# Kernel tuning notes

Measured on AMD Instinct MI355X. Metric: run time of the kernel, lower is better.

Reference implementation:

```python
import jax, jax.numpy as jnp
import numpy as np

DN = ('NCHW', 'OIHW', 'NCHW')

def _convlstm_scan(x, W, b):
    """x: [S,B,Cin,H,W]; W: [4*Co, Cin+Co, 3, 3]; b: [4*Co]. Returns all h: [S,B,Co,H,W]."""
    S, B, Cin, H, Wd = x.shape
    Co = W.shape[0] // 4
    h0 = jnp.zeros((B, Co, H, Wd), x.dtype)
    c0 = jnp.zeros((B, Co, H, Wd), x.dtype)

    def step(carry, xt):
        h, c = carry
        z = jax.lax.conv_general_dilated(
            jnp.concatenate([xt, h], axis=1), W,
            window_strides=(1, 1), padding='SAME', dimension_numbers=DN)
        z = z + b[None, :, None, None]
        i, f, o, g = jnp.split(z, 4, axis=1)
        c = jax.nn.sigmoid(f) * c + jax.nn.sigmoid(i) * jnp.tanh(g)
        h = jax.nn.sigmoid(o) * jnp.tanh(c)
        return (h, c), h

    _, outs = jax.lax.scan(step, (h0, c0), x)
    return outs


def setup_inputs() -> dict:
    key = jax.random.key(0)
    k1, k2, k3 = jax.random.split(key, 3)
    S, B, C, H, W = 16, 4, 32, 128, 128
    Co = 32
    x = jax.random.normal(k1, (S, B, C, H, W), dtype=jnp.float32)
    Wf = jax.random.normal(k2, (4 * Co, C + Co, 3, 3), dtype=jnp.float32) * 0.05
    bf = jnp.zeros((4 * Co,), dtype=jnp.float32)
    Wb = jax.random.normal(k3, (4 * Co, C + Co, 3, 3), dtype=jnp.float32) * 0.05
    bb = jnp.zeros((4 * Co,), dtype=jnp.float32)
    return {"x": x, "Wf": Wf, "bf": bf, "Wb": Wb, "bb": bb}


def reference(x, Wf, bf, Wb, bb):
    fwd_outs = _convlstm_scan(x, Wf, bf)            # [S,B,Co,H,W]
    bwd_outs = _convlstm_scan(x[::-1], Wb, bb)      # [S,B,Co,H,W] (time-reversed input)
    # Faithful to source: backward outputs concatenated WITHOUT re-flipping.
    return jnp.concatenate([fwd_outs, bwd_outs], axis=2)  # [S,B,2*Co,H,W]
```

## Files before the change

kernel.cpp:

```cpp
#include <hip/hip_runtime.h>

#define S_ 16
#define B_ 4
#define H_ 128
#define W_ 128
#define HW_ (H_ * W_)
#define NPOS 324
#define TILE_ELEMS (NPOS * 32)

typedef __attribute__((ext_vector_type(8))) _Float16 half8;
typedef __attribute__((ext_vector_type(4))) float f32x4;

__device__ __forceinline__ float sigf(float x) { return 1.f / (1.f + __expf(-x)); }
__device__ __forceinline__ float tanhf_(float x) { return 2.f / (1.f + __expf(-2.f * x)) - 1.f; }

__device__ __forceinline__ void gl2lds16(const _Float16* g, _Float16* l) {
    __builtin_amdgcn_global_load_lds(
        (const __attribute__((address_space(1))) unsigned int*)g,
        (__attribute__((address_space(3))) unsigned int*)l, 16, 0, 0);
}

__global__ void prep_pack(const float* __restrict__ Wf, const float* __restrict__ Wb,
                          _Float16* __restrict__ wpk) {
    int id = blockIdx.x * 256 + threadIdx.x;
    if (id >= 18432) return;
    int l = id & 63;
    int nf = (id >> 6) & 7;
    int ks = (id >> 9) % 18;
    int d = id / 9216;
    const float* Wsrc = d ? Wb : Wf;
    int tap = ks >> 1, half = ks & 1;
    int dy = tap / 3, dx = tap - dy * 3;
    int co = nf * 16 + (l & 15);
    _Float16* dst = wpk + (size_t)d * 73728 + ((size_t)(ks * 8 + nf) * 64 + l) * 8;
#pragma unroll
    for (int e = 0; e < 8; ++e) {
        int ci = half * 32 + (l >> 4) * 8 + e;
        dst[e] = (_Float16)Wsrc[((co * 64 + ci) * 3 + dy) * 3 + dx];
    }
}

__global__ void prep_xtiles(const float* __restrict__ x, _Float16* __restrict__ xt) {
    int id = blockIdx.x * 256 + threadIdx.x;
    if (id >= 16 * 4 * 64 * NPOS * 4) return;
    int cb = id & 3;
    int u = id >> 2;
    int pos = u % NPOS;
    int v = u / NPOS;
    int tile = v & 63;
    v >>= 6;
    int b = v & 3;
    int ts = v >> 2;
    int r = pos / 18, cc = pos - r * 18;
    int gy = (tile >> 3) * 16 + r - 1;
    int gx = (tile & 7) * 16 + cc - 1;
    bool inb = ((unsigned)gy < 128u) && ((unsigned)gx < 128u);
    const float* g = x + ((size_t)(ts * 4 + b) * 32 + cb * 8) * HW_ + (size_t)gy * W_ + gx;
    half8 vv;
#pragma unroll
    for (int e = 0; e < 8; ++e)
        vv[e] = inb ? (_Float16)g[e * HW_] : (_Float16)0.f;
    *(half8*)(xt + (size_t)u * 32 + cb * 8) = vv;
}

__device__ __forceinline__ half8 lda(const _Float16* __restrict__ base, int m, int dy,
                                     int dx, int px, int kg, int wq) {
    return *(const half8*)(base + (size_t)(((wq * 4 + m + dy) * 18) + px + dx) * 32 + kg * 8);
}
__device__ __forceinline__ half8 ldb(const _Float16* __restrict__ bw, int ks, int nf, int lane) {
    return *(const half8*)(bw + (size_t)(ks * 8 + nf) * 512 + lane * 8);
}

__global__ __launch_bounds__(256, 2)
void convlstm_step(const _Float16* __restrict__ xtiles,
                   const _Float16* __restrict__ hin,
                   _Float16* __restrict__ hout,
                   const _Float16* __restrict__ wpk,
                   const float* __restrict__ biasf, const float* __restrict__ biasb,
                   float* __restrict__ cst, float* __restrict__ out, int t) {
    const int tile = blockIdx.x;
    const int dirb = blockIdx.y;
    const int dir = dirb >> 2, b = dirb & 3;
    const int ts = dir ? (S_ - 1 - t) : t;

    const _Float16* base_x = xtiles + ((size_t)(ts * 4 + b) * 64 + tile) * TILE_ELEMS;
    const _Float16* base_h = hin + ((size_t)dirb * 64 + tile) * TILE_ELEMS;
    _Float16* hob = hout + (size_t)dirb * 64 * TILE_ELEMS;
    const _Float16* bw = wpk + (size_t)dir * 73728;
    const float* bias = dir ? biasb : biasf;
    float* cbase = cst + (size_t)dirb * 32 * HW_;
    float* outp = out + ((size_t)(t * 4 + b) * 64 + dir * 32) * HW_;

    __shared__ alignas(16) _Float16 bsh[2][8][64][8];

    const int tid = threadIdx.x;
    const int lane = tid & 63, wq = tid >> 6;
    const int px = lane & 15, kg = lane >> 4;

    f32x4 acc[4][8];
#pragma unroll
    for (int m = 0; m < 4; ++m)
#pragma unroll
        for (int nf = 0; nf < 8; ++nf) acc[m][nf] = (f32x4)(0.f);

    if (t == 0) {
#pragma unroll 1
        for (int tap = 0; tap < 9; ++tap) {
            int dy = tap / 3, dx = tap - dy * 3;
            half8 a[4];
#pragma unroll
            for (int m = 0; m < 4; ++m) a[m] = lda(base_x, m, dy, dx, px, kg, wq);
#pragma unroll
            for (int nf = 0; nf < 8; ++nf) {
                half8 bb8 = ldb(bw, tap * 2, nf, lane);
#pragma unroll
                for (int m = 0; m < 4; ++m)
                    acc[m][nf] = __builtin_amdgcn_mfma_f32_16x16x32_f16(a[m], bb8, acc[m][nf], 0, 0, 0);
            }
        }
    } else {
        half8 aP[4], aQ[4];
        {
            const _Float16* gs = bw + ((size_t)(0 * 8 + wq * 2) * 64 + lane) * 8;
            gl2lds16(gs, &bsh[0][wq * 2][0][0]);
            gl2lds16(gs + 512, &bsh[0][wq * 2 + 1][0][0]);
#pragma unroll
            for (int m = 0; m < 4; ++m) aP[m] = lda(base_x, m, 0, 0, px, kg, wq);
        }

        auto body = [&](int ks, half8(&acur)[4], half8(&anxt)[4]) {
            __syncthreads();
            if (ks < 17) {
                const int ksn = ks + 1;
                const _Float16* gs = bw + ((size_t)(ksn * 8 + wq * 2) * 64 + lane) * 8;
                gl2lds16(gs, &bsh[ksn & 1][wq * 2][0][0]);
                gl2lds16(gs + 512, &bsh[ksn & 1][wq * 2 + 1][0][0]);
                const int tapn = ksn >> 1;
                const int dyn_ = tapn / 3, dxn = tapn - dyn_ * 3;
                const _Float16* an = (ksn & 1) ? base_h : base_x;
#pragma unroll
                for (int m = 0; m < 4; ++m) anxt[m] = lda(an, m, dyn_, dxn, px, kg, wq);
            }
            const _Float16* lb = &bsh[ks & 1][0][0][0];
#pragma unroll
            for (int nf = 0; nf < 8; ++nf) {
                half8 bb8 = *(const half8*)(lb + nf * 512 + lane * 8);
#pragma unroll
                for (int m = 0; m < 4; ++m)
                    acc[m][nf] = __builtin_amdgcn_mfma_f32_16x16x32_f16(acur[m], bb8, acc[m][nf], 0, 0, 0);
            }
        };
#pragma unroll 1
        for (int ks = 0; ks < 18; ks += 2) {
            body(ks, aP, aQ);
            body(ks + 1, aQ, aP);
        }
    }

    const int q0 = px;
    const int gx0 = (tile & 7) * 16, gy0 = (tile >> 3) * 16;
    const int tx = tile & 7, ty_ = tile >> 3;
    const int lx0 = kg * 4;

    float bI[2], bF[2], bO[2], bG[2];
#pragma unroll
    for (int qs = 0; qs < 2; ++qs) {
        bI[qs] = bias[qs * 16 + q0];
        bF[qs] = bias[32 + qs * 16 + q0];
        bO[qs] = bias[64 + qs * 16 + q0];
        bG[qs] = bias[96 + qs * 16 + q0];
    }
#pragma unroll
    for (int m = 0; m < 4; ++m) {
        const int ly = wq * 4 + m;
        const int gy = gy0 + ly;
#pragma unroll
        for (int qs = 0; qs < 2; ++qs) {
            const int q = qs * 16 + q0;
            f32x4 zi = acc[m][qs], zf = acc[m][2 + qs], zo = acc[m][4 + qs], zg = acc[m][6 + qs];
            size_t off = (size_t)q * HW_ + (size_t)gy * W_ + gx0 + lx0;
            f32x4 cold = (f32x4)(0.f);
            if (t) cold = *(const f32x4*)(cbase + off);
            f32x4 cn, hn;
#pragma unroll
            for (int r = 0; r < 4; ++r) {
                float I = sigf(zi[r] + bI[qs]);
                float F = sigf(zf[r] + bF[qs]);
                float O = sigf(zo[r] + bO[qs]);
                float G = tanhf_(zg[r] + bG[qs]);
                float cnr = F * cold[r] + I * G;
                cn[r] = cnr;
                hn[r] = O * tanhf_(cnr);
            }
            *(f32x4*)(cbase + off) = cn;
            *(f32x4*)(outp + off) = hn;
#pragma unroll
            for (int r = 0; r < 4; ++r) {
                _Float16 hh = (_Float16)hn[r];
                int lx = lx0 + r;
                hob[((size_t)tile) * TILE_ELEMS + (size_t)((ly + 1) * 18 + lx + 1) * 32 + q] = hh;
                bool Le = (lx == 0) && (tx > 0);
                bool Re = (lx == 15) && (tx < 7);
                bool Te = (ly == 0) && (ty_ > 0);
                bool Be = (ly == 15) && (ty_ < 7);
                if (Le) hob[((size_t)tile - 1) * TILE_ELEMS + (size_t)((ly + 1) * 18 + 17) * 32 + q] = hh;
                if (Re) hob[((size_t)tile + 1) * TILE_ELEMS + (size_t)((ly + 1) * 18 + 0) * 32 + q] = hh;
                if (Te) hob[((size_t)tile - 8) * TILE_ELEMS + (size_t)(17 * 18 + lx + 1) * 32 + q] = hh;
                if (Be) hob[((size_t)tile + 8) * TILE_ELEMS + (size_t)(0 * 18 + lx + 1) * 32 + q] = hh;
                if (Te && Le) hob[((size_t)tile - 9) * TILE_ELEMS + (size_t)(17 * 18 + 17) * 32 + q] = hh;
                if (Te && Re) hob[((size_t)tile - 7) * TILE_ELEMS + (size_t)(17 * 18 + 0) * 32 + q] = hh;
                if (Be && Le) hob[((size_t)tile + 7) * TILE_ELEMS + (size_t)(0 * 18 + 17) * 32 + q] = hh;
                if (Be && Re) hob[((size_t)tile + 9) * TILE_ELEMS + (size_t)(0 * 18 + 0) * 32 + q] = hh;
            }
        }
    }
}

extern "C" void kernel_launch(void* const* d_in, const int* in_sizes, int n_in,
                              void* d_out, int out_size, void* d_ws, size_t ws_size,
                              hipStream_t stream) {
    const float* x  = (const float*)d_in[0];
    const float* Wf = (const float*)d_in[1];
    const float* bf = (const float*)d_in[2];
    const float* Wb = (const float*)d_in[3];
    const float* bb = (const float*)d_in[4];
    float* out = (float*)d_out;
    char* ws = (char*)d_ws;

    const size_t OFF_WPK = 0;
    const size_t OFF_XT  = 327680;
    const size_t OFF_H0  = OFF_XT + 84934656;
    const size_t OFF_H1  = OFF_H0 + 10616832;
    const size_t OFF_C   = OFF_H1 + 10616832;

    _Float16* wpk = (_Float16*)(ws + OFF_WPK);
    _Float16* xt  = (_Float16*)(ws + OFF_XT);
    _Float16* hb[2] = { (_Float16*)(ws + OFF_H0), (_Float16*)(ws + OFF_H1) };
    float* cst = (float*)(ws + OFF_C);

    hipMemsetAsync(ws + OFF_H0, 0, 2u * 10616832u, stream);

    prep_pack<<<dim3(72), dim3(256), 0, stream>>>(Wf, Wb, wpk);
    prep_xtiles<<<dim3(20736), dim3(256), 0, stream>>>(x, xt);

    for (int t = 0; t < S_; ++t) {
        convlstm_step<<<dim3(64, 8), dim3(256), 0, stream>>>(
            xt, hb[(t + 1) & 1], hb[t & 1], wpk, bf, bb, cst, out, t);
    }
}
```

Baseline: 649.9 us.

## Process x and h halves per tap together, store cell state in fp16

The main loop now runs once per tap (9 iterations) instead of once per k-slice (18). Each iteration double-buffers both the x and h weight halves and loads both A operands, which halves the number of __syncthreads barriers. The cell state buffer changes from fp32 to fp16, halving its read/write traffic at the cost of precision in the recurrent c state. Nontemporal loads in the x packing and nontemporal stores of the output are added, and the larger LDS buffer and extra A registers may reduce occupancy.

Result: slower. 683.6 us (+5.2%).

```diff
diff --git a/kernel.cpp b/kernel.cpp
--- a/kernel.cpp
+++ b/kernel.cpp
@@ -9,6 +9,7 @@
 #define TILE_ELEMS (NPOS * 32)
 
 typedef __attribute__((ext_vector_type(8))) _Float16 half8;
+typedef __attribute__((ext_vector_type(4))) _Float16 half4;
 typedef __attribute__((ext_vector_type(4))) float f32x4;
 
 __device__ __forceinline__ float sigf(float x) { return 1.f / (1.f + __expf(-x)); }
@@ -59,7 +60,7 @@
     half8 vv;
 #pragma unroll
     for (int e = 0; e < 8; ++e)
-        vv[e] = inb ? (_Float16)g[e * HW_] : (_Float16)0.f;
+        vv[e] = inb ? (_Float16)__builtin_nontemporal_load(g + e * HW_) : (_Float16)0.f;
     *(half8*)(xt + (size_t)u * 32 + cb * 8) = vv;
 }
 
@@ -77,7 +78,8 @@
                    _Float16* __restrict__ hout,
                    const _Float16* __restrict__ wpk,
                    const float* __restrict__ biasf, const float* __restrict__ biasb,
-                   float* __restrict__ cst, float* __restrict__ out, int t) {
+                   _Float16* __restrict__ cst,
+                   float* __restrict__ out, int t) {
     const int tile = blockIdx.x;
     const int dirb = blockIdx.y;
     const int dir = dirb >> 2, b = dirb & 3;
@@ -88,10 +90,10 @@
     _Float16* hob = hout + (size_t)dirb * 64 * TILE_ELEMS;
     const _Float16* bw = wpk + (size_t)dir * 73728;
     const float* bias = dir ? biasb : biasf;
-    float* cbase = cst + (size_t)dirb * 32 * HW_;
+    _Float16* cbase = cst + (size_t)dirb * 32 * HW_;
     float* outp = out + ((size_t)(t * 4 + b) * 64 + dir * 32) * HW_;
 
-    __shared__ alignas(16) _Float16 bsh[2][8][64][8];
+    __shared__ alignas(16) _Float16 bsh[2][2][8][64][8];
 
     const int tid = threadIdx.x;
     const int lane = tid & 63, wq = tid >> 6;
@@ -119,41 +121,55 @@
             }
         }
     } else {
-        half8 aP[4], aQ[4];
+        half8 aP[2][4], aQ[2][4];
         {
-            const _Float16* gs = bw + ((size_t)(0 * 8 + wq * 2) * 64 + lane) * 8;
-            gl2lds16(gs, &bsh[0][wq * 2][0][0]);
-            gl2lds16(gs + 512, &bsh[0][wq * 2 + 1][0][0]);
-#pragma unroll
-            for (int m = 0; m < 4; ++m) aP[m] = lda(base_x, m, 0, 0, px, kg, wq);
-        }
-
-        auto body = [&](int ks, half8(&acur)[4], half8(&anxt)[4]) {
+#pragma unroll
+            for (int j = 0; j < 4; ++j) {
+                int f = wq * 4 + j;
+                int hf = f >> 3, nf = f & 7;
+                gl2lds16(bw + (size_t)(hf * 8 + nf) * 512 + lane * 8, &bsh[0][hf][nf][0][0]);
+            }
+#pragma unroll
+            for (int m = 0; m < 4; ++m) {
+                aP[0][m] = lda(base_x, m, 0, 0, px, kg, wq);
+                aP[1][m] = lda(base_h, m, 0, 0, px, kg, wq);
+            }
+        }
+
+        auto body = [&](int tap, half8(&acur)[2][4], half8(&anxt)[2][4]) {
             __syncthreads();
-            if (ks < 17) {
-                const int ksn = ks + 1;
-                const _Float16* gs = bw + ((size_t)(ksn * 8 + wq * 2) * 64 + lane) * 8;
-                gl2lds16(gs, &bsh[ksn & 1][wq * 2][0][0]);
-                gl2lds16(gs + 512, &bsh[ksn & 1][wq * 2 + 1][0][0]);
-                const int tapn = ksn >> 1;
-                const int dyn_ = tapn / 3, dxn = tapn - dyn_ * 3;
-                const _Float16* an = (ksn & 1) ? base_h : base_x;
-#pragma unroll
-                for (int m = 0; m < 4; ++m) anxt[m] = lda(an, m, dyn_, dxn, px, kg, wq);
-            }
-            const _Float16* lb = &bsh[ks & 1][0][0][0];
-#pragma unroll
-            for (int nf = 0; nf < 8; ++nf) {
-                half8 bb8 = *(const half8*)(lb + nf * 512 + lane * 8);
-#pragma unroll
-                for (int m = 0; m < 4; ++m)
-                    acc[m][nf] = __builtin_amdgcn_mfma_f32_16x16x32_f16(acur[m], bb8, acc[m][nf], 0, 0, 0);
+            if (tap < 8) {
+                const int tn = tap + 1;
+                const int dyn_ = tn / 3, dxn = tn - dyn_ * 3;
+#pragma unroll
+                for (int j = 0; j < 4; ++j) {
+                    int f = wq * 4 + j;
+                    int hf = f >> 3, nf = f & 7;
+                    gl2lds16(bw + (size_t)((tn * 2 + hf) * 8 + nf) * 512 + lane * 8,
+                             &bsh[tn & 1][hf][nf][0][0]);
+                }
+#pragma unroll
+                for (int m = 0; m < 4; ++m) {
+                    anxt[0][m] = lda(base_x, m, dyn_, dxn, px, kg, wq);
+                    anxt[1][m] = lda(base_h, m, dyn_, dxn, px, kg, wq);
+                }
+            }
+            const _Float16* lb = &bsh[tap & 1][0][0][0][0];
+#pragma unroll
+            for (int hf = 0; hf < 2; ++hf) {
+#pragma unroll
+                for (int nf = 0; nf < 8; ++nf) {
+                    half8 bb8 = *(const half8*)(lb + (size_t)(hf * 8 + nf) * 512 + lane * 8);
+#pragma unroll
+                    for (int m = 0; m < 4; ++m)
+                        acc[m][nf] = __builtin_amdgcn_mfma_f32_16x16x32_f16(acur[hf][m], bb8, acc[m][nf], 0, 0, 0);
+                }
             }
         };
 #pragma unroll 1
-        for (int ks = 0; ks < 18; ks += 2) {
-            body(ks, aP, aQ);
-            body(ks + 1, aQ, aP);
+        for (int tap = 0; tap < 9; tap += 2) {
+            body(tap, aP, aQ);
+            if (tap + 1 < 9) body(tap + 1, aQ, aP);
         }
     }
 
@@ -179,21 +195,22 @@
             const int q = qs * 16 + q0;
             f32x4 zi = acc[m][qs], zf = acc[m][2 + qs], zo = acc[m][4 + qs], zg = acc[m][6 + qs];
             size_t off = (size_t)q * HW_ + (size_t)gy * W_ + gx0 + lx0;
-            f32x4 cold = (f32x4)(0.f);
-            if (t) cold = *(const f32x4*)(cbase + off);
-            f32x4 cn, hn;
+            half4 cold4 = (half4)((_Float16)0.f);
+            if (t) cold4 = *(const half4*)(cbase + off);
+            half4 cn4;
+            f32x4 hn;
 #pragma unroll
             for (int r = 0; r < 4; ++r) {
                 float I = sigf(zi[r] + bI[qs]);
                 float F = sigf(zf[r] + bF[qs]);
                 float O = sigf(zo[r] + bO[qs]);
                 float G = tanhf_(zg[r] + bG[qs]);
-                float cnr = F * cold[r] + I * G;
-                cn[r] = cnr;
+                float cnr = F * (float)cold4[r] + I * G;
+                cn4[r] = (_Float16)cnr;
                 hn[r] = O * tanhf_(cnr);
             }
-            *(f32x4*)(cbase + off) = cn;
-            *(f32x4*)(outp + off) = hn;
+            *(half4*)(cbase + off) = cn4;
+            __builtin_nontemporal_store(hn, (f32x4*)(outp + off));
 #pragma unroll
             for (int r = 0; r < 4; ++r) {
                 _Float16 hh = (_Float16)hn[r];
@@ -236,7 +253,7 @@
     _Float16* wpk = (_Float16*)(ws + OFF_WPK);
     _Float16* xt  = (_Float16*)(ws + OFF_XT);
     _Float16* hb[2] = { (_Float16*)(ws + OFF_H0), (_Float16*)(ws + OFF_H1) };
-    float* cst = (float*)(ws + OFF_C);
+    _Float16* cst = (_Float16*)(ws + OFF_C);
 
     hipMemsetAsync(ws + OFF_H0, 0, 2u * 10616832u, stream);
 
```

## Stage h in LDS for vectorized halo writes; store cell state as fp16

Applied to the files above, without the earlier changes.

The epilogue now writes new h values into a shared-memory staging buffer, then copies the tile interior and its halo edges and corners out to the neighbour tiles with 16-byte vector stores. This replaces the scattered 2-byte global writes used before. The cell state is kept in fp16 instead of fp32, halving its read and write traffic at some cost in accuracy. Nontemporal loads and stores are also used for the input packing and for the output writes. The extra LDS buffer and barrier may lower occupancy.

New measurement: 680.1 us. 1.05x slower.

```diff
diff --git a/kernel.cpp b/kernel.cpp
--- a/kernel.cpp
+++ b/kernel.cpp
@@ -7,8 +7,10 @@
 #define HW_ (H_ * W_)
 #define NPOS 324
 #define TILE_ELEMS (NPOS * 32)
+#define HS 40
 
 typedef __attribute__((ext_vector_type(8))) _Float16 half8;
+typedef __attribute__((ext_vector_type(4))) _Float16 half4;
 typedef __attribute__((ext_vector_type(4))) float f32x4;
 
 __device__ __forceinline__ float sigf(float x) { return 1.f / (1.f + __expf(-x)); }
@@ -59,7 +61,7 @@
     half8 vv;
 #pragma unroll
     for (int e = 0; e < 8; ++e)
-        vv[e] = inb ? (_Float16)g[e * HW_] : (_Float16)0.f;
+        vv[e] = inb ? (_Float16)__builtin_nontemporal_load(g + e * HW_) : (_Float16)0.f;
     *(half8*)(xt + (size_t)u * 32 + cb * 8) = vv;
 }
 
@@ -77,7 +79,8 @@
                    _Float16* __restrict__ hout,
                    const _Float16* __restrict__ wpk,
                    const float* __restrict__ biasf, const float* __restrict__ biasb,
-                   float* __restrict__ cst, float* __restrict__ out, int t) {
+                   _Float16* __restrict__ cst,
+                   float* __restrict__ out, int t) {
     const int tile = blockIdx.x;
     const int dirb = blockIdx.y;
     const int dir = dirb >> 2, b = dirb & 3;
@@ -88,10 +91,11 @@
     _Float16* hob = hout + (size_t)dirb * 64 * TILE_ELEMS;
     const _Float16* bw = wpk + (size_t)dir * 73728;
     const float* bias = dir ? biasb : biasf;
-    float* cbase = cst + (size_t)dirb * 32 * HW_;
+    _Float16* cbase = cst + (size_t)dirb * 32 * HW_;
     float* outp = out + ((size_t)(t * 4 + b) * 64 + dir * 32) * HW_;
 
     __shared__ alignas(16) _Float16 bsh[2][8][64][8];
+    __shared__ alignas(16) _Float16 hsh[256 * HS];
 
     const int tid = threadIdx.x;
     const int lane = tid & 63, wq = tid >> 6;
@@ -127,7 +131,6 @@
 #pragma unroll
             for (int m = 0; m < 4; ++m) aP[m] = lda(base_x, m, 0, 0, px, kg, wq);
         }
-
         auto body = [&](int ks, half8(&acur)[4], half8(&anxt)[4]) {
             __syncthreads();
             if (ks < 17) {
@@ -179,40 +182,68 @@
             const int q = qs * 16 + q0;
             f32x4 zi = acc[m][qs], zf = acc[m][2 + qs], zo = acc[m][4 + qs], zg = acc[m][6 + qs];
             size_t off = (size_t)q * HW_ + (size_t)gy * W_ + gx0 + lx0;
-            f32x4 cold = (f32x4)(0.f);
-            if (t) cold = *(const f32x4*)(cbase + off);
-            f32x4 cn, hn;
+            half4 cold4 = (half4)((_Float16)0.f);
+            if (t) cold4 = *(const half4*)(cbase + off);
+            half4 cn4;
+            f32x4 hn;
 #pragma unroll
             for (int r = 0; r < 4; ++r) {
                 float I = sigf(zi[r] + bI[qs]);
                 float F = sigf(zf[r] + bF[qs]);
                 float O = sigf(zo[r] + bO[qs]);
                 float G = tanhf_(zg[r] + bG[qs]);
-                float cnr = F * cold[r] + I * G;
-                cn[r] = cnr;
+                float cnr = F * (float)cold4[r] + I * G;
+                cn4[r] = (_Float16)cnr;
                 hn[r] = O * tanhf_(cnr);
             }
-            *(f32x4*)(cbase + off) = cn;
-            *(f32x4*)(outp + off) = hn;
-#pragma unroll
-            for (int r = 0; r < 4; ++r) {
-                _Float16 hh = (_Float16)hn[r];
-                int lx = lx0 + r;
-                hob[((size_t)tile) * TILE_ELEMS + (size_t)((ly + 1) * 18 + lx + 1) * 32 + q] = hh;
-                bool Le = (lx == 0) && (tx > 0);
-                bool Re = (lx == 15) && (tx < 7);
-                bool Te = (ly == 0) && (ty_ > 0);
-                bool Be = (ly == 15) && (ty_ < 7);
-                if (Le) hob[((size_t)tile - 1) * TILE_ELEMS + (size_t)((ly + 1) * 18 + 17) * 32 + q] = hh;
-                if (Re) hob[((size_t)tile + 1) * TILE_ELEMS + (size_t)((ly + 1) * 18 + 0) * 32 + q] = hh;
-                if (Te) hob[((size_t)tile - 8) * TILE_ELEMS + (size_t)(17 * 18 + lx + 1) * 32 + q] = hh;
-                if (Be) hob[((size_t)tile + 8) * TILE_ELEMS + (size_t)(0 * 18 + lx + 1) * 32 + q] = hh;
-                if (Te && Le) hob[((size_t)tile - 9) * TILE_ELEMS + (size_t)(17 * 18 + 17) * 32 + q] = hh;
-                if (Te && Re) hob[((size_t)tile - 7) * TILE_ELEMS + (size_t)(17 * 18 + 0) * 32 + q] = hh;
-                if (Be && Le) hob[((size_t)tile + 7) * TILE_ELEMS + (size_t)(0 * 18 + 17) * 32 + q] = hh;
-                if (Be && Re) hob[((size_t)tile + 9) * TILE_ELEMS + (size_t)(0 * 18 + 0) * 32 + q] = hh;
-            }
-        }
+            *(half4*)(cbase + off) = cn4;
+            __builtin_nontemporal_store(hn, (f32x4*)(outp + off));
+#pragma unroll
+            for (int r = 0; r < 4; ++r)
+                hsh[(ly * 16 + lx0 + r) * HS + q] = (_Float16)hn[r];
+        }
+    }
+    __syncthreads();
+
+    _Float16* ownb = hob + (size_t)tile * TILE_ELEMS;
+#pragma unroll 1
+    for (int c = tid; c < 1024; c += 256) {
+        int pxi = c >> 2, c8 = c & 3;
+        int ly = pxi >> 4, lx = pxi & 15;
+        *(half8*)(ownb + (size_t)((ly + 1) * 18 + lx + 1) * 32 + c8 * 8) =
+            *(const half8*)(hsh + pxi * HS + c8 * 8);
+    }
+    {
+        const int sid = tid >> 6;
+        const int st = tid & 63;
+        const int rr = st >> 2, c8 = st & 3;
+        if (sid == 0 && tx > 0)
+            *(half8*)(hob + (size_t)(tile - 1) * TILE_ELEMS + (size_t)((rr + 1) * 18 + 17) * 32 + c8 * 8) =
+                *(const half8*)(hsh + (rr * 16 + 0) * HS + c8 * 8);
+        if (sid == 1 && tx < 7)
+            *(half8*)(hob + (size_t)(tile + 1) * TILE_ELEMS + (size_t)((rr + 1) * 18 + 0) * 32 + c8 * 8) =
+                *(const half8*)(hsh + (rr * 16 + 15) * HS + c8 * 8);
+        if (sid == 2 && ty_ > 0)
+            *(half8*)(hob + (size_t)(tile - 8) * TILE_ELEMS + (size_t)(17 * 18 + rr + 1) * 32 + c8 * 8) =
+                *(const half8*)(hsh + (0 * 16 + rr) * HS + c8 * 8);
+        if (sid == 3 && ty_ < 7)
+            *(half8*)(hob + (size_t)(tile + 8) * TILE_ELEMS + (size_t)(0 * 18 + rr + 1) * 32 + c8 * 8) =
+                *(const half8*)(hsh + (15 * 16 + rr) * HS + c8 * 8);
+    }
+    if (tid < 16) {
+        const int cid = tid >> 2, c8 = tid & 3;
+        if (cid == 0 && tx > 0 && ty_ > 0)
+            *(half8*)(hob + (size_t)(tile - 9) * TILE_ELEMS + (size_t)(17 * 18 + 17) * 32 + c8 * 8) =
+                *(const half8*)(hsh + 0 * HS + c8 * 8);
+        if (cid == 1 && tx < 7 && ty_ > 0)
+            *(half8*)(hob + (size_t)(tile - 7) * TILE_ELEMS + (size_t)(17 * 18 + 0) * 32 + c8 * 8) =
+                *(const half8*)(hsh + 15 * HS + c8 * 8);
+        if (cid == 2 && tx > 0 && ty_ < 7)
+            *(half8*)(hob + (size_t)(tile + 7) * TILE_ELEMS + (size_t)(0 * 18 + 17) * 32 + c8 * 8) =
+                *(const half8*)(hsh + 240 * HS + c8 * 8);
+        if (cid == 3 && tx < 7 && ty_ < 7)
+            *(half8*)(hob + (size_t)(tile + 9) * TILE_ELEMS + (size_t)(0 * 18 + 0) * 32 + c8 * 8) =
+                *(const half8*)(hsh + 255 * HS + c8 * 8);
     }
 }
 
@@ -236,7 +267,7 @@
     _Float16* wpk = (_Float16*)(ws + OFF_WPK);
     _Float16* xt  = (_Float16*)(ws + OFF_XT);
     _Float16* hb[2] = { (_Float16*)(ws + OFF_H0), (_Float16*)(ws + OFF_H1) };
-    float* cst = (float*)(ws + OFF_C);
+    _Float16* cst = (_Float16*)(ws + OFF_C);
 
     hipMemsetAsync(ws + OFF_H0, 0, 2u * 10616832u, stream);
 
```
